# Kernel tuning notes

Hardware: AMD Instinct MI355X
Metric: run time of the kernel (lower is better)

## Reference

```python
import jax, jax.numpy as jnp
import numpy as np

N_HEAD = 16
ROPE_BASE = 10000.0


def rope_cache(T, dim):
    half = dim // 2
    inv_freq = 1.0 / (ROPE_BASE ** (jnp.arange(half, dtype=jnp.float32) / half))
    freqs = jnp.arange(T, dtype=jnp.float32)[:, None] * inv_freq[None, :]  # [T, half]
    cos = jnp.repeat(jnp.cos(freqs), 2, axis=-1)  # [T, dim]
    sin = jnp.repeat(jnp.sin(freqs), 2, axis=-1)
    return cos, sin


def apply_rope(x, cos, sin):
    # x: [B, H, T, hd]; cos/sin: [T, hd] broadcast over B,H
    x1 = x[..., ::2]
    x2 = x[..., 1::2]
    x_rot = jnp.stack([-x2, x1], axis=-1).reshape(x.shape)
    return x * cos + x_rot * sin


def setup_inputs() -> dict:
    key = jax.random.key(0)
    k1, k2, k3, k4 = jax.random.split(key, 4)
    C = 1024
    x = jax.random.normal(k1, (2, 2048, C), jnp.float32)
    w_qkv = jax.random.normal(k2, (3 * C, C), jnp.float32) * 0.02
    w_out = jax.random.normal(k3, (C, C), jnp.float32) * 0.02
    b_out = jax.random.normal(k4, (C,), jnp.float32) * 0.02
    return {"x": x, "w_qkv": w_qkv, "w_out": w_out, "b_out": b_out}


def reference(x, w_qkv, w_out, b_out):
    B, T, C = x.shape
    H = N_HEAD
    hd = C // H
    qkv = x @ w_qkv.T                              # [B, T, 3C]
    qkv = qkv.reshape(B, T, 3, H, hd).transpose(2, 0, 3, 1, 4)  # [3, B, H, T, hd]
    q, k, v = qkv[0], qkv[1], qkv[2]
    cos, sin = rope_cache(T, hd)
    q = apply_rope(q, cos, sin)
    k = apply_rope(k, cos, sin)
    scale = hd ** (-0.5)
    scores = jnp.einsum('bhqd,bhkd->bhqk', q, k) * scale       # [B, H, T, T]
    causal = jnp.tril(jnp.ones((T, T), dtype=bool))
    scores = jnp.where(causal, scores, jnp.float32(-jnp.inf))
    att = jax.nn.softmax(scores, axis=-1)
    out = jnp.einsum('bhqk,bhkd->bhqd', att, v)                # [B, H, T, hd]
    out = out.transpose(0, 2, 1, 3).reshape(B, T, C)
    return out @ w_out.T + b_out
```

## Files before the change

### kernel.cpp

```cpp
#include <hip/hip_runtime.h>
#include <math.h>

namespace {

typedef __attribute__((ext_vector_type(8))) short s16x8;
typedef __attribute__((ext_vector_type(4))) float f32x4;
typedef unsigned int u32;
typedef unsigned short u16;

constexpr int B_ = 2;
constexpr int T_ = 2048;
constexpr int C_ = 1024;
constexpr int H_ = 16;
constexpr float L2E = 1.44269504088896340736f;

__device__ inline u16 f2bf(float x) {
    __bf16 h = (__bf16)x;
    return __builtin_bit_cast(u16, h);
}
__device__ inline u32 packbf2(float a, float b) {
    return (u32)f2bf(a) | ((u32)f2bf(b) << 16);
}
__device__ inline void gload_lds16(const void* g, void* lds) {
    __builtin_amdgcn_global_load_lds(
        (const __attribute__((address_space(1))) unsigned int*)g,
        (__attribute__((address_space(3))) unsigned int*)lds, 16, 0, 0);
}

#define VMW(n) asm volatile("s_waitcnt vmcnt(" #n ")" ::: "memory")
#define LGW0() asm volatile("s_waitcnt lgkmcnt(0)" ::: "memory")
#define BARRIER() do { __builtin_amdgcn_s_barrier(); asm volatile("" ::: "memory"); } while (0)

__global__ __launch_bounds__(256) void tab_k(float2* __restrict__ cs) {
    int idx = blockIdx.x * 256 + threadIdx.x;
    int t = idx >> 5, i = idx & 31;
    float inv = 1.0f / powf(10000.0f, (float)i / 32.0f);
    float ang = (float)t * inv;
    cs[idx] = make_float2(cosf(ang), sinf(ang));
}

__global__ __launch_bounds__(256)
void cvt_k(const float4* __restrict__ x, const float4* __restrict__ wq,
           const float4* __restrict__ wo, uint2* __restrict__ xb,
           uint2* __restrict__ wqb, uint2* __restrict__ wob) {
    int i = blockIdx.x * 256 + threadIdx.x;
    const float4* s;
    uint2* d;
    int j;
    if (i < 1048576) { s = x; d = xb; j = i; }
    else if (i < 1048576 + 786432) { s = wq; d = wqb; j = i - 1048576; }
    else { s = wo; d = wob; j = i - (1048576 + 786432); }
    float4 v = s[j];
    d[j] = make_uint2(packbf2(v.x, v.y), packbf2(v.z, v.w));
}

__global__ __launch_bounds__(256)
void qkv_mfma_k(const u16* __restrict__ xb, const u16* __restrict__ wqb,
                const float2* __restrict__ cs, u16* __restrict__ qb,
                u16* __restrict__ kb, u16* __restrict__ vt) {
    __shared__ char lds[49152];
    char* const b0 = lds;
    char* const b1 = lds + 16384;
    char* const b2 = lds + 32768;
    const int tid = threadIdx.x;
    const int w = tid >> 6, lane = tid & 63;
    const int c = lane & 15, g = lane >> 4;
    const int n0 = blockIdx.x * 128, m0 = blockIdx.y * 128;
    const int wr = w >> 1, wc = w & 1;

    f32x4 acc[4][4];
#pragma unroll
    for (int i = 0; i < 4; ++i)
#pragma unroll
        for (int j = 0; j < 4; ++j) acc[i][j] = (f32x4){0.f, 0.f, 0.f, 0.f};

    const u16* Ab = xb + (size_t)m0 * C_;
    const u16* Bb = wqb + (size_t)n0 * C_;
    const int srow = tid >> 2, sslot = tid & 3;

    auto stage = [&](int t, char* base) {
        int k0 = t * 32;
#pragma unroll
        for (int call = 0; call < 2; ++call) {
            int r = call * 64 + srow;
            int ds = sslot ^ ((r >> 1) & 3);
            gload_lds16(Ab + (size_t)r * C_ + k0 + ds * 8, base + call * 4096 + w * 1024);
            gload_lds16(Bb + (size_t)r * C_ + k0 + ds * 8, base + 8192 + call * 4096 + w * 1024);
        }
    };
    auto compute = [&](const char* base) {
        s16x8 aF[4], bF[4];
#pragma unroll
        for (int mf = 0; mf < 4; ++mf) {
            int row = wr * 64 + mf * 16 + c;
            aF[mf] = *(const s16x8*)(base + row * 64 + ((g ^ ((row >> 1) & 3)) * 16));
        }
#pragma unroll
        for (int nf = 0; nf < 4; ++nf) {
            int row = wc * 64 + nf * 16 + c;
            bF[nf] = *(const s16x8*)(base + 8192 + row * 64 + ((g ^ ((row >> 1) & 3)) * 16));
        }
#pragma unroll
        for (int mf = 0; mf < 4; ++mf)
#pragma unroll
            for (int nf = 0; nf < 4; ++nf)
                acc[mf][nf] = __builtin_amdgcn_mfma_f32_16x16x32_bf16(aF[mf], bF[nf], acc[mf][nf], 0, 0, 0);
    };

    stage(0, b0);
    stage(1, b1);
#pragma unroll 1
    for (int t = 0; t < 30; t += 3) {
        VMW(4); BARRIER(); stage(t + 2, b2); compute(b0); LGW0();
        VMW(4); BARRIER(); stage(t + 3, b0); compute(b1); LGW0();
        VMW(4); BARRIER(); stage(t + 4, b1); compute(b2); LGW0();
    }
    VMW(4); BARRIER(); compute(b0); LGW0();
    VMW(0); BARRIER(); compute(b1);

    const int sec = n0 >> 10;
    const int h = ((n0 & 1023) >> 6) + wc;
    const int b = m0 >> 11;
    const int t0w = (m0 & 2047) + wr * 64;
    const int bh = b * H_ + h;
    if (sec < 2) {
        u16* dst = (sec == 0) ? qb : kb;
        const float qs = (sec == 0) ? 0.125f : 1.0f;
#pragma unroll
        for (int nf = 0; nf < 4; ++nf) {
            int d = nf * 16 + c;
            int ibase = nf * 8 + (c >> 1);
#pragma unroll
            for (int mf = 0; mf < 4; ++mf) {
#pragma unroll
                for (int r = 0; r < 4; ++r) {
                    int t = t0w + mf * 16 + g * 4 + r;
                    float own = acc[mf][nf][r];
                    float partner = __shfl_xor(own, 1);
                    float2 csv = cs[t * 32 + ibase];
                    float rot = (d & 1) ? (own * csv.x + partner * csv.y)
                                        : (own * csv.x - partner * csv.y);
                    rot *= qs;
                    float rothi = __shfl_xor(rot, 1);
                    if (!(d & 1))
                        *(u32*)(dst + ((size_t)bh * T_ + t) * 64 + d) = packbf2(rot, rothi);
                }
            }
        }
    } else {
#pragma unroll
        for (int nf = 0; nf < 4; ++nf) {
            int d = nf * 16 + c;
#pragma unroll
            for (int mf = 0; mf < 4; ++mf) {
                int tb = t0w + mf * 16 + g * 4;
                u32 lo = packbf2(acc[mf][nf][0], acc[mf][nf][1]);
                u32 hi = packbf2(acc[mf][nf][2], acc[mf][nf][3]);
                *(uint2*)(vt + ((size_t)bh * 64 + d) * T_ + tb) = make_uint2(lo, hi);
            }
        }
    }
}

__global__ __launch_bounds__(256)
void flash_mfma_k(const u16* __restrict__ qb, const u16* __restrict__ kb,
                  const u16* __restrict__ vt, u16* __restrict__ attb) {
    __shared__ char lds[32768];
    char* Qs = lds;
    char* Ks = lds + 8192;
    char* Vs = lds + 16384;
    char* Ps = lds + 24576;
    const int tid = threadIdx.x, w = tid >> 6, lane = tid & 63;
    const int c = lane & 15, g = lane >> 4;
    const int bh = blockIdx.x;
    const int qi = 31 - blockIdx.y;
    const int q0 = qi * 64, q0w = q0 + w * 16;
    const u16* Qg = qb + ((size_t)bh * T_ + q0) * 64;
    const u16* Kg = kb + (size_t)bh * T_ * 64;
    const u16* Vg = vt + (size_t)bh * 64 * T_;

#pragma unroll
    for (int call = 0; call < 2; ++call) {
        int row = call * 32 + (tid >> 3);
        int ds = (tid & 7) ^ (row & 7);
        gload_lds16(Qg + (size_t)row * 64 + ds * 8, Qs + call * 4096 + w * 1024);
    }
    __syncthreads();

    s16x8 bQ[2];
#pragma unroll
    for (int kc = 0; kc < 2; ++kc) {
        int row = w * 16 + c;
        bQ[kc] = *(const s16x8*)(Qs + row * 128 + (((kc * 4 + g) ^ (row & 7)) * 16));
    }

    float m_ = -INFINITY, l_ = 0.f;
    f32x4 accO[4];
#pragma unroll
    for (int j = 0; j < 4; ++j) accO[j] = (f32x4){0.f, 0.f, 0.f, 0.f};

    const int nt = qi + 1;
    for (int kt = 0; kt < nt; ++kt) {
        __syncthreads();
        {
            int row = tid >> 3, slot = tid & 7;
#pragma unroll
            for (int call = 0; call < 2; ++call) {
                int r = call * 32 + row;
                int ds = slot ^ (r & 7);
                gload_lds16(Kg + (size_t)(kt * 64 + r) * 64 + ds * 8, Ks + call * 4096 + w * 1024);
                gload_lds16(Vg + (size_t)r * T_ + kt * 64 + ds * 8, Vs + call * 4096 + w * 1024);
            }
        }
        __syncthreads();

        f32x4 S[4];
#pragma unroll
        for (int mf = 0; mf < 4; ++mf) S[mf] = (f32x4){0.f, 0.f, 0.f, 0.f};
        s16x8 aK[4][2];
#pragma unroll
        for (int mf = 0; mf < 4; ++mf)
#pragma unroll
            for (int kc = 0; kc < 2; ++kc) {
                int row = mf * 16 + c;
                aK[mf][kc] = *(const s16x8*)(Ks + row * 128 + (((kc * 4 + g) ^ (row & 7)) * 16));
            }
#pragma unroll
        for (int kc = 0; kc < 2; ++kc)
#pragma unroll
            for (int mf = 0; mf < 4; ++mf)
                S[mf] = __builtin_amdgcn_mfma_f32_16x16x32_bf16(aK[mf][kc], bQ[kc], S[mf], 0, 0, 0);

        if (kt == qi) {
#pragma unroll
            for (int mf = 0; mf < 4; ++mf)
#pragma unroll
                for (int r = 0; r < 4; ++r) {
                    int kvg = kt * 64 + mf * 16 + g * 4 + r;
                    if (kvg > q0w + c) S[mf][r] = -INFINITY;
                }
        }

        float mx = -INFINITY;
#pragma unroll
        for (int mf = 0; mf < 4; ++mf)
#pragma unroll
            for (int r = 0; r < 4; ++r) mx = fmaxf(mx, S[mf][r]);
        mx = fmaxf(mx, __shfl_xor(mx, 16));
        mx = fmaxf(mx, __shfl_xor(mx, 32));
        float alpha = 1.0f;
        if (!__all(mx - m_ <= 8.0f)) {
            float mnew = fmaxf(m_, mx);
            alpha = exp2f((m_ - mnew) * L2E);
            m_ = mnew;
#pragma unroll
            for (int r = 0; r < 4; ++r) {
                float ar = __shfl(alpha, g * 4 + r);
#pragma unroll
                for (int nd = 0; nd < 4; ++nd) accO[nd][r] *= ar;
            }
        }
        float sum = 0.f;
#pragma unroll
        for (int mf = 0; mf < 4; ++mf)
#pragma unroll
            for (int r = 0; r < 4; ++r) {
                float p = exp2f((S[mf][r] - m_) * L2E);
                S[mf][r] = p;
                sum += p;
            }
        sum += __shfl_xor(sum, 16);
        sum += __shfl_xor(sum, 32);
        l_ = l_ * alpha + sum;

#pragma unroll
        for (int mf = 0; mf < 4; ++mf)
#pragma unroll
            for (int p2 = 0; p2 < 2; ++p2) {
                u32 v = packbf2(S[mf][2 * p2], S[mf][2 * p2 + 1]);
                int off = (mf * 16 + g * 4 + p2 * 2) * 2;
                *(u32*)(Ps + w * 2048 + c * 128 + (off ^ ((c & 7) << 4))) = v;
            }
        __threadfence_block();

        s16x8 aP[2], bV[4][2];
#pragma unroll
        for (int kc = 0; kc < 2; ++kc)
            aP[kc] = *(const s16x8*)(Ps + w * 2048 + c * 128 + (((kc * 4 + g) ^ (c & 7)) * 16));
#pragma unroll
        for (int nd = 0; nd < 4; ++nd)
#pragma unroll
            for (int kc = 0; kc < 2; ++kc) {
                int row = nd * 16 + c;
                bV[nd][kc] = *(const s16x8*)(Vs + row * 128 + (((kc * 4 + g) ^ (row & 7)) * 16));
            }
#pragma unroll
        for (int kc = 0; kc < 2; ++kc)
#pragma unroll
            for (int nd = 0; nd < 4; ++nd)
                accO[nd] = __builtin_amdgcn_mfma_f32_16x16x32_bf16(aP[kc], bV[nd][kc], accO[nd], 0, 0, 0);
    }

    const int hh = bh & 15;
    const int bb = bh >> 4;
#pragma unroll
    for (int r = 0; r < 4; ++r) {
        float linv = 1.0f / __shfl(l_, g * 4 + r);
        int t = q0w + g * 4 + r;
        size_t rowb = ((size_t)bb * T_ + t) * C_ + hh * 64;
#pragma unroll
        for (int nd = 0; nd < 4; ++nd)
            attb[rowb + nd * 16 + c] = f2bf(accO[nd][r] * linv);
    }
}

__global__ __launch_bounds__(256)
void proj_mfma_k(const u16* __restrict__ attb, const u16* __restrict__ wob,
                 const float* __restrict__ bias, float* __restrict__ out) {
    __shared__ char lds[49152];
    char* const b0 = lds;
    char* const b1 = lds + 16384;
    char* const b2 = lds + 32768;
    const int tid = threadIdx.x;
    const int w = tid >> 6, lane = tid & 63;
    const int c = lane & 15, g = lane >> 4;
    const int n0 = blockIdx.x * 128, m0 = blockIdx.y * 128;
    const int wr = w >> 1, wc = w & 1;

    f32x4 acc[4][4];
#pragma unroll
    for (int i = 0; i < 4; ++i)
#pragma unroll
        for (int j = 0; j < 4; ++j) acc[i][j] = (f32x4){0.f, 0.f, 0.f, 0.f};

    const u16* Ab = attb + (size_t)m0 * C_;
    const u16* Bb = wob + (size_t)n0 * C_;
    const int srow = tid >> 2, sslot = tid & 3;

    auto stage = [&](int t, char* base) {
        int k0 = t * 32;
#pragma unroll
        for (int call = 0; call < 2; ++call) {
            int r = call * 64 + srow;
            int ds = sslot ^ ((r >> 1) & 3);
            gload_lds16(Ab + (size_t)r * C_ + k0 + ds * 8, base + call * 4096 + w * 1024);
            gload_lds16(Bb + (size_t)r * C_ + k0 + ds * 8, base + 8192 + call * 4096 + w * 1024);
        }
    };
    auto compute = [&](const char* base) {
        s16x8 aF[4], bF[4];
#pragma unroll
        for (int mf = 0; mf < 4; ++mf) {
            int row = wr * 64 + mf * 16 + c;
            aF[mf] = *(const s16x8*)(base + row * 64 + ((g ^ ((row >> 1) & 3)) * 16));
        }
#pragma unroll
        for (int nf = 0; nf < 4; ++nf) {
            int row = wc * 64 + nf * 16 + c;
            bF[nf] = *(const s16x8*)(base + 8192 + row * 64 + ((g ^ ((row >> 1) & 3)) * 16));
        }
#pragma unroll
        for (int mf = 0; mf < 4; ++mf)
#pragma unroll
            for (int nf = 0; nf < 4; ++nf)
                acc[mf][nf] = __builtin_amdgcn_mfma_f32_16x16x32_bf16(aF[mf], bF[nf], acc[mf][nf], 0, 0, 0);
    };

    stage(0, b0);
    stage(1, b1);
#pragma unroll 1
    for (int t = 0; t < 30; t += 3) {
        VMW(4); BARRIER(); stage(t + 2, b2); compute(b0); LGW0();
        VMW(4); BARRIER(); stage(t + 3, b0); compute(b1); LGW0();
        VMW(4); BARRIER(); stage(t + 4, b1); compute(b2); LGW0();
    }
    VMW(4); BARRIER(); compute(b0); LGW0();
    VMW(0); BARRIER(); compute(b1);

#pragma unroll
    for (int nf = 0; nf < 4; ++nf) {
        int n = n0 + wc * 64 + nf * 16 + c;
        float bv = bias[n];
#pragma unroll
        for (int mf = 0; mf < 4; ++mf)
#pragma unroll
            for (int r = 0; r < 4; ++r) {
                int mrow = m0 + wr * 64 + mf * 16 + g * 4 + r;
                out[(size_t)mrow * C_ + n] = acc[mf][nf][r] + bv;
            }
    }
}

}

extern "C" void kernel_launch(void* const* d_in, const int* in_sizes, int n_in,
                              void* d_out, int out_size, void* d_ws, size_t ws_size,
                              hipStream_t stream) {
    const float* x     = (const float*)d_in[0];
    const float* w_qkv = (const float*)d_in[1];
    const float* w_out = (const float*)d_in[2];
    const float* b_out = (const float*)d_in[3];
    float* out = (float*)d_out;

    char* ws = (char*)d_ws;
    float2* cs = (float2*)ws;
    u16* xb   = (u16*)(ws + 524288);
    u16* wqb  = (u16*)(ws + 524288 + 8388608);
    u16* wob  = (u16*)(ws + 524288 + 8388608 + 6291456);
    u16* qb   = (u16*)(ws + 17301504);
    u16* kb   = (u16*)(ws + 25690112);
    u16* vt   = (u16*)(ws + 34078720);
    u16* attb = (u16*)(ws + 42467328);

    tab_k<<<256, 256, 0, stream>>>(cs);
    cvt_k<<<8192, 256, 0, stream>>>((const float4*)x, (const float4*)w_qkv,
                                    (const float4*)w_out, (uint2*)xb, (uint2*)wqb, (uint2*)wob);
    qkv_mfma_k<<<dim3(24, 32), 256, 0, stream>>>(xb, wqb, cs, qb, kb, vt);
    flash_mfma_k<<<dim3(32, 32), 256, 0, stream>>>(qb, kb, vt, attb);
    proj_mfma_k<<<dim3(8, 32), 256, 0, stream>>>(attb, wob, b_out, out);
}
```

Measured before the change: 204.5 us.

## Rewrite QKV GEMM as 256x256 tile, 8-wave ping-pong schedule

Replaces the 128x128 tile, 4-wave, triple-buffered QKV projection GEMM with a 256x256 tile run by 8 waves. It uses BK=64 double-buffered half-tiles in 128KB of dynamic LDS and an interleaved load/compute schedule with s_setprio and sched_barrier. The aim is more operand reuse per byte loaded and better overlap of global-to-LDS loads with MFMA work. In exchange it uses larger LDS and register footprints and launches only 192 blocks, which may underfill the GPU's CUs.

```diff
diff --git a/kernel.cpp b/kernel.cpp
--- a/kernel.cpp
+++ b/kernel.cpp
@@ -30,6 +30,9 @@
 #define VMW(n) asm volatile("s_waitcnt vmcnt(" #n ")" ::: "memory")
 #define LGW0() asm volatile("s_waitcnt lgkmcnt(0)" ::: "memory")
 #define BARRIER() do { __builtin_amdgcn_s_barrier(); asm volatile("" ::: "memory"); } while (0)
+#define SB0() __builtin_amdgcn_sched_barrier(0)
+#define PRIO1() __builtin_amdgcn_s_setprio(1)
+#define PRIO0() __builtin_amdgcn_s_setprio(0)
 
 __global__ __launch_bounds__(256) void tab_k(float2* __restrict__ cs) {
     int idx = blockIdx.x * 256 + threadIdx.x;
@@ -54,75 +57,203 @@
     d[j] = make_uint2(packbf2(v.x, v.y), packbf2(v.z, v.w));
 }
 
-__global__ __launch_bounds__(256)
+__global__ __launch_bounds__(512, 2)
 void qkv_mfma_k(const u16* __restrict__ xb, const u16* __restrict__ wqb,
                 const float2* __restrict__ cs, u16* __restrict__ qb,
                 u16* __restrict__ kb, u16* __restrict__ vt) {
-    __shared__ char lds[49152];
-    char* const b0 = lds;
-    char* const b1 = lds + 16384;
-    char* const b2 = lds + 32768;
+    extern __shared__ char lds[];
     const int tid = threadIdx.x;
     const int w = tid >> 6, lane = tid & 63;
     const int c = lane & 15, g = lane >> 4;
-    const int n0 = blockIdx.x * 128, m0 = blockIdx.y * 128;
-    const int wr = w >> 1, wc = w & 1;
-
-    f32x4 acc[4][4];
-#pragma unroll
-    for (int i = 0; i < 4; ++i)
+    const int n0 = blockIdx.x * 256, m0 = blockIdx.y * 256;
+    const int wr = w >> 2, wc = w & 3;
+
+    f32x4 acc[8][4];
+#pragma unroll
+    for (int i = 0; i < 8; ++i)
 #pragma unroll
         for (int j = 0; j < 4; ++j) acc[i][j] = (f32x4){0.f, 0.f, 0.f, 0.f};
 
     const u16* Ab = xb + (size_t)m0 * C_;
     const u16* Bb = wqb + (size_t)n0 * C_;
-    const int srow = tid >> 2, sslot = tid & 3;
-
-    auto stage = [&](int t, char* base) {
-        int k0 = t * 32;
+    const int srow = tid >> 3, sslot = tid & 7;
+
+    auto stA = [&](int t, int hf) {
+        char* base = lds + (((t & 1) * 2 + hf) << 14);
+        const u16* src = Ab + (size_t)(hf * 128) * C_ + t * 64;
 #pragma unroll
         for (int call = 0; call < 2; ++call) {
-            int r = call * 64 + srow;
-            int ds = sslot ^ ((r >> 1) & 3);
-            gload_lds16(Ab + (size_t)r * C_ + k0 + ds * 8, base + call * 4096 + w * 1024);
-            gload_lds16(Bb + (size_t)r * C_ + k0 + ds * 8, base + 8192 + call * 4096 + w * 1024);
+            int row = call * 64 + srow;
+            int s = sslot ^ (row & 7);
+            gload_lds16(src + (size_t)row * C_ + s * 8, base + call * 8192 + w * 1024);
         }
     };
-    auto compute = [&](const char* base) {
-        s16x8 aF[4], bF[4];
-#pragma unroll
-        for (int mf = 0; mf < 4; ++mf) {
-            int row = wr * 64 + mf * 16 + c;
-            aF[mf] = *(const s16x8*)(base + row * 64 + ((g ^ ((row >> 1) & 3)) * 16));
-        }
-#pragma unroll
-        for (int nf = 0; nf < 4; ++nf) {
-            int row = wc * 64 + nf * 16 + c;
-            bF[nf] = *(const s16x8*)(base + 8192 + row * 64 + ((g ^ ((row >> 1) & 3)) * 16));
-        }
-#pragma unroll
-        for (int mf = 0; mf < 4; ++mf)
-#pragma unroll
-            for (int nf = 0; nf < 4; ++nf)
-                acc[mf][nf] = __builtin_amdgcn_mfma_f32_16x16x32_bf16(aF[mf], bF[nf], acc[mf][nf], 0, 0, 0);
+    auto stB = [&](int t, int hf) {
+        char* base = lds + 65536 + (((t & 1) * 2 + hf) << 14);
+        const u16* src = Bb + (size_t)(hf * 128) * C_ + t * 64;
+#pragma unroll
+        for (int call = 0; call < 2; ++call) {
+            int row = call * 64 + srow;
+            int s = sslot ^ (row & 7);
+            gload_lds16(src + (size_t)row * C_ + s * 8, base + call * 8192 + w * 1024);
+        }
     };
-
-    stage(0, b0);
-    stage(1, b1);
+    auto ldA = [&](int P, int mrep, int kh) -> s16x8 {
+        const char* base = lds + ((P * 2 + wr) << 14);
+        int row = mrep * 16 + c;
+        return *(const s16x8*)(base + row * 128 + (((kh * 4 + g) ^ (row & 7)) * 16));
+    };
+    auto ldB = [&](int P, int nrep, int kh) -> s16x8 {
+        int rowg = wc * 64 + nrep * 16 + c;
+        int hf = rowg >> 7, row = rowg & 127;
+        const char* base = lds + 65536 + ((P * 2 + hf) << 14);
+        return *(const s16x8*)(base + row * 128 + (((kh * 4 + g) ^ (row & 7)) * 16));
+    };
+
+    s16x8 aA[4][2], bB0[2][2], bB1[2][2];
+
+    stA(0, 0); stA(0, 1); stB(0, 0); stB(0, 1); stB(1, 0); stB(1, 1);
+    VMW(4); BARRIER();
+
 #pragma unroll 1
-    for (int t = 0; t < 30; t += 3) {
-        VMW(4); BARRIER(); stage(t + 2, b2); compute(b0); LGW0();
-        VMW(4); BARRIER(); stage(t + 3, b0); compute(b1); LGW0();
-        VMW(4); BARRIER(); stage(t + 4, b1); compute(b2); LGW0();
-    }
-    VMW(4); BARRIER(); compute(b0); LGW0();
-    VMW(0); BARRIER(); compute(b1);
+    for (int i = 0; i < 8; ++i) {
+        const int tb_ = 2 * i + 1;
+        const bool nl = (i < 7);
+#pragma unroll
+        for (int mm = 0; mm < 4; ++mm)
+#pragma unroll
+            for (int kh = 0; kh < 2; ++kh) aA[mm][kh] = ldA(0, mm, kh);
+#pragma unroll
+        for (int nn = 0; nn < 2; ++nn)
+#pragma unroll
+            for (int kh = 0; kh < 2; ++kh) bB0[nn][kh] = ldB(0, nn, kh);
+        stA(tb_, 0);
+        BARRIER(); LGW0(); SB0();
+        PRIO1();
+#pragma unroll
+        for (int kh = 0; kh < 2; ++kh)
+#pragma unroll
+            for (int mm = 0; mm < 4; ++mm)
+#pragma unroll
+                for (int nn = 0; nn < 2; ++nn)
+                    acc[mm][nn] = __builtin_amdgcn_mfma_f32_16x16x32_bf16(aA[mm][kh], bB0[nn][kh], acc[mm][nn], 0, 0, 0);
+        PRIO0();
+        BARRIER();
+#pragma unroll
+        for (int nn = 0; nn < 2; ++nn)
+#pragma unroll
+            for (int kh = 0; kh < 2; ++kh) bB1[nn][kh] = ldB(0, 2 + nn, kh);
+        stA(tb_, 1);
+        BARRIER(); LGW0(); SB0();
+        PRIO1();
+#pragma unroll
+        for (int kh = 0; kh < 2; ++kh)
+#pragma unroll
+            for (int mm = 0; mm < 4; ++mm)
+#pragma unroll
+                for (int nn = 0; nn < 2; ++nn)
+                    acc[mm][2 + nn] = __builtin_amdgcn_mfma_f32_16x16x32_bf16(aA[mm][kh], bB1[nn][kh], acc[mm][2 + nn], 0, 0, 0);
+        PRIO0();
+        BARRIER();
+#pragma unroll
+        for (int mm = 0; mm < 4; ++mm)
+#pragma unroll
+            for (int kh = 0; kh < 2; ++kh) aA[mm][kh] = ldA(0, 4 + mm, kh);
+        if (nl) stB(2 * i + 2, 0);
+        BARRIER(); LGW0(); SB0();
+        PRIO1();
+#pragma unroll
+        for (int kh = 0; kh < 2; ++kh)
+#pragma unroll
+            for (int mm = 0; mm < 4; ++mm)
+#pragma unroll
+                for (int nn = 0; nn < 2; ++nn)
+                    acc[4 + mm][nn] = __builtin_amdgcn_mfma_f32_16x16x32_bf16(aA[mm][kh], bB0[nn][kh], acc[4 + mm][nn], 0, 0, 0);
+        PRIO0();
+        BARRIER();
+        if (nl) { stB(2 * i + 2, 1); VMW(4); } else { VMW(0); }
+        BARRIER(); SB0();
+        PRIO1();
+#pragma unroll
+        for (int kh = 0; kh < 2; ++kh)
+#pragma unroll
+            for (int mm = 0; mm < 4; ++mm)
+#pragma unroll
+                for (int nn = 0; nn < 2; ++nn)
+                    acc[4 + mm][2 + nn] = __builtin_amdgcn_mfma_f32_16x16x32_bf16(aA[mm][kh], bB1[nn][kh], acc[4 + mm][2 + nn], 0, 0, 0);
+        PRIO0();
+        BARRIER();
+#pragma unroll
+        for (int mm = 0; mm < 4; ++mm)
+#pragma unroll
+            for (int kh = 0; kh < 2; ++kh) aA[mm][kh] = ldA(1, mm, kh);
+#pragma unroll
+        for (int nn = 0; nn < 2; ++nn)
+#pragma unroll
+            for (int kh = 0; kh < 2; ++kh) bB0[nn][kh] = ldB(1, nn, kh);
+        if (nl) stA(2 * i + 2, 0);
+        BARRIER(); LGW0(); SB0();
+        PRIO1();
+#pragma unroll
+        for (int kh = 0; kh < 2; ++kh)
+#pragma unroll
+            for (int mm = 0; mm < 4; ++mm)
+#pragma unroll
+                for (int nn = 0; nn < 2; ++nn)
+                    acc[mm][nn] = __builtin_amdgcn_mfma_f32_16x16x32_bf16(aA[mm][kh], bB0[nn][kh], acc[mm][nn], 0, 0, 0);
+        PRIO0();
+        BARRIER();
+#pragma unroll
+        for (int nn = 0; nn < 2; ++nn)
+#pragma unroll
+            for (int kh = 0; kh < 2; ++kh) bB1[nn][kh] = ldB(1, 2 + nn, kh);
+        if (nl) stA(2 * i + 2, 1);
+        BARRIER(); LGW0(); SB0();
+        PRIO1();
+#pragma unroll
+        for (int kh = 0; kh < 2; ++kh)
+#pragma unroll
+            for (int mm = 0; mm < 4; ++mm)
+#pragma unroll
+                for (int nn = 0; nn < 2; ++nn)
+                    acc[mm][2 + nn] = __builtin_amdgcn_mfma_f32_16x16x32_bf16(aA[mm][kh], bB1[nn][kh], acc[mm][2 + nn], 0, 0, 0);
+        PRIO0();
+        BARRIER();
+#pragma unroll
+        for (int mm = 0; mm < 4; ++mm)
+#pragma unroll
+            for (int kh = 0; kh < 2; ++kh) aA[mm][kh] = ldA(1, 4 + mm, kh);
+        if (nl) stB(2 * i + 3, 0);
+        BARRIER(); LGW0(); SB0();
+        PRIO1();
+#pragma unroll
+        for (int kh = 0; kh < 2; ++kh)
+#pragma unroll
+            for (int mm = 0; mm < 4; ++mm)
+#pragma unroll
+                for (int nn = 0; nn < 2; ++nn)
+                    acc[4 + mm][nn] = __builtin_amdgcn_mfma_f32_16x16x32_bf16(aA[mm][kh], bB0[nn][kh], acc[4 + mm][nn], 0, 0, 0);
+        PRIO0();
+        BARRIER();
+        if (nl) { stB(2 * i + 3, 1); VMW(4); }
+        BARRIER(); SB0();
+        PRIO1();
+#pragma unroll
+        for (int kh = 0; kh < 2; ++kh)
+#pragma unroll
+            for (int mm = 0; mm < 4; ++mm)
+#pragma unroll
+                for (int nn = 0; nn < 2; ++nn)
+                    acc[4 + mm][2 + nn] = __builtin_amdgcn_mfma_f32_16x16x32_bf16(aA[mm][kh], bB1[nn][kh], acc[4 + mm][2 + nn], 0, 0, 0);
+        PRIO0();
+        BARRIER();
+    }
 
     const int sec = n0 >> 10;
-    const int h = ((n0 & 1023) >> 6) + wc;
+    const int hD = ((n0 & 1023) >> 6) + wc;
     const int b = m0 >> 11;
-    const int t0w = (m0 & 2047) + wr * 64;
-    const int bh = b * H_ + h;
+    const int t0w = (m0 & 2047) + wr * 128;
+    const int bh = b * H_ + hD;
     if (sec < 2) {
         u16* dst = (sec == 0) ? qb : kb;
         const float qs = (sec == 0) ? 0.125f : 1.0f;
@@ -131,7 +262,7 @@
             int d = nf * 16 + c;
             int ibase = nf * 8 + (c >> 1);
 #pragma unroll
-            for (int mf = 0; mf < 4; ++mf) {
+            for (int mf = 0; mf < 8; ++mf) {
 #pragma unroll
                 for (int r = 0; r < 4; ++r) {
                     int t = t0w + mf * 16 + g * 4 + r;
@@ -152,11 +283,11 @@
         for (int nf = 0; nf < 4; ++nf) {
             int d = nf * 16 + c;
 #pragma unroll
-            for (int mf = 0; mf < 4; ++mf) {
-                int tb = t0w + mf * 16 + g * 4;
+            for (int mf = 0; mf < 8; ++mf) {
+                int tb2 = t0w + mf * 16 + g * 4;
                 u32 lo = packbf2(acc[mf][nf][0], acc[mf][nf][1]);
                 u32 hi = packbf2(acc[mf][nf][2], acc[mf][nf][3]);
-                *(uint2*)(vt + ((size_t)bh * 64 + d) * T_ + tb) = make_uint2(lo, hi);
+                *(uint2*)(vt + ((size_t)bh * 64 + d) * T_ + tb2) = make_uint2(lo, hi);
             }
         }
     }
@@ -412,10 +543,13 @@
     u16* vt   = (u16*)(ws + 34078720);
     u16* attb = (u16*)(ws + 42467328);
 
+    (void)hipFuncSetAttribute((const void*)qkv_mfma_k,
+                              hipFuncAttributeMaxDynamicSharedMemorySize, 131072);
+
     tab_k<<<256, 256, 0, stream>>>(cs);
     cvt_k<<<8192, 256, 0, stream>>>((const float4*)x, (const float4*)w_qkv,
                                     (const float4*)w_out, (uint2*)xb, (uint2*)wqb, (uint2*)wob);
-    qkv_mfma_k<<<dim3(24, 32), 256, 0, stream>>>(xb, wqb, cs, qb, kb, vt);
+    qkv_mfma_k<<<dim3(12, 16), 512, 131072, stream>>>(xb, wqb, cs, qb, kb, vt);
     flash_mfma_k<<<dim3(32, 32), 256, 0, stream>>>(qb, kb, vt, attb);
     proj_mfma_k<<<dim3(8, 32), 256, 0, stream>>>(attb, wob, b_out, out);
 }
```

Result: no change. 206.5 us (+1.0%).
